# Kernel optimization log

Measured on AMD Instinct MI355X. Metric: run time of the kernel, lower is better.

The kernel has to match this reference:

```python
import jax, jax.numpy as jnp
import numpy as np

B, T, TWO_H = 64, 512, 1024  # batch, prev decoding steps, 2*hidden_dim


def setup_inputs() -> dict:
    key = jax.random.key(0)
    k1, k2, k3 = jax.random.split(key, 3)
    h_d_t = jax.random.normal(k1, (B, TWO_H), dtype=jnp.float32)
    prev_h_dec = jax.random.normal(k2, (B, T, TWO_H), dtype=jnp.float32)
    # nn.Bilinear(2H, 2H, attn_dim=1) weight, trunc_norm_init_std ~ 1e-4 typical
    W = jax.random.normal(k3, (1, TWO_H, TWO_H), dtype=jnp.float32) * 1e-4
    return {"h_d_t": h_d_t, "prev_h_dec": prev_h_dec, "W": W}


def reference(h_d_t, prev_h_dec, W):
    # Bilinear score: s[b,t] = h_d_t[b] @ W[0] @ prev_h_dec[b,t]
    q = jnp.einsum('bd,de->be', h_d_t, W[0])          # (B, 2H) -- one small GEMM
    attn_score = jnp.einsum('be,bte->bt', q, prev_h_dec)  # (B, T)
    alpha_t = jax.nn.softmax(attn_score, axis=1)      # (B, T)
    ct_d = jnp.einsum('bt,btd->bd', alpha_t, prev_h_dec)  # (B, 2H)
    new_prev = jnp.concatenate([prev_h_dec, h_d_t[:, None, :]], axis=1)  # (B, T+1, 2H)
    return (ct_d, new_prev)
```

## Files before the change

### kernel.cpp

```cpp
#include <hip/hip_runtime.h>
#include <math.h>

#define BB    64
#define TT    512
#define TWOH  1024
#define WPB   4
#define TCB   WPB
#define NCHUNK (TT / TCB)
#define KSPLIT 4
#define NP_STRIDE ((TT + 1) * TWOH)

typedef float vfloat4 __attribute__((ext_vector_type(4)));


__device__ __forceinline__ void gload_lds16(const float* g, float* l) {
    __builtin_amdgcn_global_load_lds(
        (const __attribute__((address_space(1))) unsigned int*)g,
        (__attribute__((address_space(3))) unsigned int*)l,
        16, 0, 0);
}

__global__ __launch_bounds__(256) void k_qgemm(const float* __restrict__ h,
                                               const float* __restrict__ W,
                                               float* __restrict__ qpart) {
    const int tid = threadIdx.x;
    const int e   = blockIdx.x * 256 + tid;
    const int b   = blockIdx.y;
    const int k   = blockIdx.z;
    const int d0  = k * (TWOH / KSPLIT);

    __shared__ float sh[TWOH / KSPLIT];
    sh[tid] = h[b * TWOH + d0 + tid];
    __syncthreads();

    const float* __restrict__ Wp = W + (size_t)d0 * TWOH + e;
    float acc = 0.f;
    #pragma unroll 16
    for (int d = 0; d < TWOH / KSPLIT; ++d)
        acc = fmaf(sh[d], Wp[(size_t)d * TWOH], acc);

    qpart[((size_t)k * BB + b) * TWOH + e] = acc;
}

__global__ __launch_bounds__(256) void k_qreduce(const float* __restrict__ qpart,
                                                 float* __restrict__ q) {
    const int b   = blockIdx.x;
    const int tid = threadIdx.x;
    const vfloat4* __restrict__ qp = (const vfloat4*)qpart;
    const vfloat4 s = qp[(0 * BB + b) * 256 + tid]
                    + qp[(1 * BB + b) * 256 + tid]
                    + qp[(2 * BB + b) * 256 + tid]
                    + qp[(3 * BB + b) * 256 + tid];
    ((vfloat4*)(q + (size_t)b * TWOH))[tid] = s;
}

__global__ __launch_bounds__(256, 8) void k_scores_ct(const float* __restrict__ prev,
                                                      const float* __restrict__ q,
                                                      float* __restrict__ out_np,
                                                      float* __restrict__ ws_m,
                                                      float* __restrict__ ws_l,
                                                      float* __restrict__ ws_ct) {
    const int tid  = threadIdx.x;
    const int lane = tid & 63;
    const int wid  = tid >> 6;
    const int c    = blockIdx.x;
    const int b    = blockIdx.y;
    const int t    = c * TCB + wid;

    __shared__ float srow[WPB][TWOH];
    __shared__ float sscore[WPB];

    const float* gbase = prev + ((size_t)b * TT + t) * TWOH;
    #pragma unroll
    for (int j = 0; j < 4; ++j)
        gload_lds16(gbase + j * 256 + lane * 4, &srow[wid][j * 256]);

    const vfloat4* __restrict__ qv = (const vfloat4*)(q + (size_t)b * TWOH);
    const vfloat4 q0 = qv[lane];
    const vfloat4 q1 = qv[64 + lane];
    const vfloat4 q2 = qv[128 + lane];
    const vfloat4 q3 = qv[192 + lane];

    asm volatile("s_waitcnt vmcnt(0)" ::: "memory");
    __builtin_amdgcn_sched_barrier(0);

    const vfloat4* sr = (const vfloat4*)&srow[wid][0];
    vfloat4* __restrict__ nprow =
        (vfloat4*)(out_np + (size_t)b * NP_STRIDE + (size_t)t * TWOH) + lane;
    const vfloat4 v0 = sr[lane];
    const vfloat4 v1 = sr[64 + lane];
    const vfloat4 v2 = sr[128 + lane];
    const vfloat4 v3 = sr[192 + lane];
    nprow[0]   = v0;
    nprow[64]  = v1;
    nprow[128] = v2;
    nprow[192] = v3;
    float d0 = v0.x * q0.x; d0 = fmaf(v0.y, q0.y, d0);
    d0 = fmaf(v0.z, q0.z, d0); d0 = fmaf(v0.w, q0.w, d0);
    float d1 = v1.x * q1.x; d1 = fmaf(v1.y, q1.y, d1);
    d1 = fmaf(v1.z, q1.z, d1); d1 = fmaf(v1.w, q1.w, d1);
    float d2 = v2.x * q2.x; d2 = fmaf(v2.y, q2.y, d2);
    d2 = fmaf(v2.z, q2.z, d2); d2 = fmaf(v2.w, q2.w, d2);
    float d3 = v3.x * q3.x; d3 = fmaf(v3.y, q3.y, d3);
    d3 = fmaf(v3.z, q3.z, d3); d3 = fmaf(v3.w, q3.w, d3);
    float pd = (d0 + d1) + (d2 + d3);
    #pragma unroll
    for (int off = 32; off > 0; off >>= 1)
        pd += __shfl_xor(pd, off, 64);
    if (lane == 0) sscore[wid] = pd;
    __syncthreads();

    const float s0 = sscore[0], s1 = sscore[1], s2 = sscore[2], s3 = sscore[3];
    const float M  = fmaxf(fmaxf(s0, s1), fmaxf(s2, s3));
    const float a0 = __expf(s0 - M);
    const float a1 = __expf(s1 - M);
    const float a2 = __expf(s2 - M);
    const float a3 = __expf(s3 - M);
    const float L  = (a0 + a1) + (a2 + a3);

    const vfloat4 x0 = ((const vfloat4*)&srow[0][0])[tid];
    const vfloat4 x1 = ((const vfloat4*)&srow[1][0])[tid];
    const vfloat4 x2 = ((const vfloat4*)&srow[2][0])[tid];
    const vfloat4 x3 = ((const vfloat4*)&srow[3][0])[tid];
    vfloat4 o;
    o.x = fmaf(a3, x3.x, fmaf(a2, x2.x, fmaf(a1, x1.x, a0 * x0.x)));
    o.y = fmaf(a3, x3.y, fmaf(a2, x2.y, fmaf(a1, x1.y, a0 * x0.y)));
    o.z = fmaf(a3, x3.z, fmaf(a2, x2.z, fmaf(a1, x1.z, a0 * x0.z)));
    o.w = fmaf(a3, x3.w, fmaf(a2, x2.w, fmaf(a1, x1.w, a0 * x0.w)));
    ((vfloat4*)(ws_ct + ((size_t)b * NCHUNK + c) * TWOH))[tid] = o;
    if (tid == 0) {
        ws_m[b * NCHUNK + c] = M;
        ws_l[b * NCHUNK + c] = L;
    }
}

__global__ __launch_bounds__(256) void k_finalize(const float* __restrict__ h,
                                                  const float* __restrict__ ws_m,
                                                  const float* __restrict__ ws_l,
                                                  const float* __restrict__ ws_ct,
                                                  float* __restrict__ out_ct,
                                                  float* __restrict__ out_np) {
    const int tid = threadIdx.x;
    const int e   = blockIdx.x * 256 + tid;
    const int b   = blockIdx.y;

    const float* __restrict__ wm = ws_m + b * NCHUNK;
    const float* __restrict__ wl = ws_l + b * NCHUNK;

    float M = -INFINITY;
    #pragma unroll 32
    for (int i = 0; i < NCHUNK; ++i) M = fmaxf(M, wm[i]);

    const float* __restrict__ cp = ws_ct + (size_t)b * NCHUNK * TWOH + e;
    float L = 0.f;
    float acc = 0.f;
    #pragma unroll 32
    for (int i = 0; i < NCHUNK; ++i) {
        const float ce = __expf(wm[i] - M);
        L   = fmaf(ce, wl[i], L);
        acc = fmaf(ce, cp[(size_t)i * TWOH], acc);
    }
    out_ct[b * TWOH + e] = acc * (1.0f / L);

    out_np[(size_t)b * NP_STRIDE + (size_t)TT * TWOH + e] = h[b * TWOH + e];
}

extern "C" void kernel_launch(void* const* d_in, const int* in_sizes, int n_in,
                              void* d_out, int out_size, void* d_ws, size_t ws_size,
                              hipStream_t stream) {
    const float* h    = (const float*)d_in[0];
    const float* prev = (const float*)d_in[1];
    const float* W    = (const float*)d_in[2];
    float* out    = (float*)d_out;
    float* out_ct = out;
    float* out_np = out + BB * TWOH;

    float* qpart = (float*)d_ws;
    float* qred  = qpart + KSPLIT * BB * TWOH;
    float* wsm   = qred + BB * TWOH;
    float* wsl   = wsm + BB * NCHUNK;
    float* wsc   = wsl + BB * NCHUNK;

    k_qgemm<<<dim3(4, BB, KSPLIT), 256, 0, stream>>>(h, W, qpart);
    k_qreduce<<<dim3(BB), 256, 0, stream>>>(qpart, qred);
    k_scores_ct<<<dim3(NCHUNK, BB), 256, 0, stream>>>(prev, qred, out_np, wsm, wsl, wsc);
    k_finalize<<<dim3(4, BB), 256, 0, stream>>>(h, wsm, wsl, wsc, out_ct, out_np);
}
```

Baseline: 276.5 us.

## Move prev_h_dec copy to 2D memcpy and drop q GEMM split-K reduction

Removes the per-row copy of prev_h_dec into the concatenated output from the scores kernel and does it with a separate hipMemcpy2DAsync (DMA/blit) after scoring. The q GEMM is no longer split-K, which eliminates the qreduce kernel and its launch. The cost is that prev (128MB) is now read twice, once by the scores kernel and once by the memcpy, instead of once. In exchange the copy may run through a better-optimized copy path, and the scores kernel writes less. The un-split GEMM also has fewer blocks and a longer serial loop over d.

```diff
diff --git a/kernel.cpp b/kernel.cpp
--- a/kernel.cpp
+++ b/kernel.cpp
@@ -7,7 +7,6 @@
 #define WPB   4
 #define TCB   WPB
 #define NCHUNK (TT / TCB)
-#define KSPLIT 4
 #define NP_STRIDE ((TT + 1) * TWOH)
 
 typedef float vfloat4 __attribute__((ext_vector_type(4)));
@@ -22,41 +21,26 @@
 
 __global__ __launch_bounds__(256) void k_qgemm(const float* __restrict__ h,
                                                const float* __restrict__ W,
-                                               float* __restrict__ qpart) {
+                                               float* __restrict__ q) {
     const int tid = threadIdx.x;
     const int e   = blockIdx.x * 256 + tid;
     const int b   = blockIdx.y;
-    const int k   = blockIdx.z;
-    const int d0  = k * (TWOH / KSPLIT);
 
-    __shared__ float sh[TWOH / KSPLIT];
-    sh[tid] = h[b * TWOH + d0 + tid];
+    __shared__ float sh[TWOH];
+    ((vfloat4*)sh)[tid] = ((const vfloat4*)(h + (size_t)b * TWOH))[tid];
     __syncthreads();
 
-    const float* __restrict__ Wp = W + (size_t)d0 * TWOH + e;
+    const float* __restrict__ Wp = W + e;
     float acc = 0.f;
     #pragma unroll 16
-    for (int d = 0; d < TWOH / KSPLIT; ++d)
+    for (int d = 0; d < TWOH; ++d)
         acc = fmaf(sh[d], Wp[(size_t)d * TWOH], acc);
 
-    qpart[((size_t)k * BB + b) * TWOH + e] = acc;
-}
-
-__global__ __launch_bounds__(256) void k_qreduce(const float* __restrict__ qpart,
-                                                 float* __restrict__ q) {
-    const int b   = blockIdx.x;
-    const int tid = threadIdx.x;
-    const vfloat4* __restrict__ qp = (const vfloat4*)qpart;
-    const vfloat4 s = qp[(0 * BB + b) * 256 + tid]
-                    + qp[(1 * BB + b) * 256 + tid]
-                    + qp[(2 * BB + b) * 256 + tid]
-                    + qp[(3 * BB + b) * 256 + tid];
-    ((vfloat4*)(q + (size_t)b * TWOH))[tid] = s;
+    q[(size_t)b * TWOH + e] = acc;
 }
 
 __global__ __launch_bounds__(256, 8) void k_scores_ct(const float* __restrict__ prev,
                                                       const float* __restrict__ q,
-                                                      float* __restrict__ out_np,
                                                       float* __restrict__ ws_m,
                                                       float* __restrict__ ws_l,
                                                       float* __restrict__ ws_ct) {
@@ -85,16 +69,10 @@
     __builtin_amdgcn_sched_barrier(0);
 
     const vfloat4* sr = (const vfloat4*)&srow[wid][0];
-    vfloat4* __restrict__ nprow =
-        (vfloat4*)(out_np + (size_t)b * NP_STRIDE + (size_t)t * TWOH) + lane;
     const vfloat4 v0 = sr[lane];
     const vfloat4 v1 = sr[64 + lane];
     const vfloat4 v2 = sr[128 + lane];
     const vfloat4 v3 = sr[192 + lane];
-    nprow[0]   = v0;
-    nprow[64]  = v1;
-    nprow[128] = v2;
-    nprow[192] = v3;
     float d0 = v0.x * q0.x; d0 = fmaf(v0.y, q0.y, d0);
     d0 = fmaf(v0.z, q0.z, d0); d0 = fmaf(v0.w, q0.w, d0);
     float d1 = v1.x * q1.x; d1 = fmaf(v1.y, q1.y, d1);
@@ -175,14 +153,18 @@
     float* out_ct = out;
     float* out_np = out + BB * TWOH;
 
-    float* qpart = (float*)d_ws;
-    float* qred  = qpart + KSPLIT * BB * TWOH;
-    float* wsm   = qred + BB * TWOH;
-    float* wsl   = wsm + BB * NCHUNK;
-    float* wsc   = wsl + BB * NCHUNK;
+    float* q   = (float*)d_ws;
+    float* wsm = q + BB * TWOH;
+    float* wsl = wsm + BB * NCHUNK;
+    float* wsc = wsl + BB * NCHUNK;
 
-    k_qgemm<<<dim3(4, BB, KSPLIT), 256, 0, stream>>>(h, W, qpart);
-    k_qreduce<<<dim3(BB), 256, 0, stream>>>(qpart, qred);
-    k_scores_ct<<<dim3(NCHUNK, BB), 256, 0, stream>>>(prev, qred, out_np, wsm, wsl, wsc);
-    k_finalize<<<dim3(4, BB), 256, 0, stream>>>(h, wsm, wsl, wsc, out_ct, out_np);
+    k_qgemm    <<<dim3(4, BB),      256, 0, stream>>>(h, W, q);
+    k_scores_ct<<<dim3(NCHUNK, BB), 256, 0, stream>>>(prev, q, wsm, wsl, wsc);
+
+    hipMemcpy2DAsync(out_np, (size_t)NP_STRIDE * sizeof(float),
+                     prev,   (size_t)TT * TWOH * sizeof(float),
+                     (size_t)TT * TWOH * sizeof(float), BB,
+                     hipMemcpyDeviceToDevice, stream);
+
+    k_finalize <<<dim3(4, BB),      256, 0, stream>>>(h, wsm, wsl, wsc, out_ct, out_np);
 }
```

Result: slower. 325.6 us (+17.8%).
